# Optimization experiments

Hardware: AMD Instinct MI355X
Metric: run time of the kernel (lower is better)

## Reference

```python
import jax, jax.numpy as jnp
import numpy as np

N, G, F, K, E = 8192, 128, 128, 4, 1


def setup_inputs() -> dict:
    key = jax.random.key(0)
    k1, k2, k3, k4 = jax.random.split(key, 4)
    x = jax.random.normal(k1, (N, G), dtype=jnp.float32)
    # Scale GSO so repeated powers S^k stay numerically tame (spectral norm ~2).
    S = jax.random.normal(k2, (E, N, N), dtype=jnp.float32) / jnp.sqrt(jnp.float32(N))
    weight = jax.random.normal(k3, (F, E, K, G), dtype=jnp.float32)
    bias = jax.random.normal(k4, (F, 1), dtype=jnp.float32)
    return {"x": x, "S": S, "weight": weight, "bias": bias, "ind": 0}


def reference(x, S, weight, bias, ind):
    # x: [N, G] -> torch forward reshapes to [B=1, G, N]
    del ind  # GSO selector; the dense GSO S is passed in directly
    K_taps = weight.shape[2]
    Ef = S.shape[0]
    xk = jnp.broadcast_to(x.T[None, None], (1, Ef, x.shape[1], x.shape[0]))  # [B,E,G,N]
    zs = [xk]
    for _ in range(1, K_taps):  # fixed small K-hop power iteration
        xk = jnp.matmul(xk, S[None])  # [B,E,G,N] @ [1,E,N,N] -> [B,E,G,N]
        zs.append(xk)
    z = jnp.stack(zs, axis=2)  # [B,E,K,G,N]
    # y_f = sum_{e,k,g} h[f,e,k,g] * (S^k x)_g  + b_f
    y = jnp.einsum('bekgn,fekg->bfn', z, weight) + bias  # [B,F,N]
    return y
```

## Files before the change

### kernel.cpp

```cpp
#include <hip/hip_runtime.h>

typedef _Float16 f16;
typedef _Float16 f16x8 __attribute__((ext_vector_type(8)));
typedef float f32x4 __attribute__((ext_vector_type(4)));
typedef unsigned int u32;

#define NN 8192
#define GG 128
#define NSPLIT 16

typedef __attribute__((address_space(3))) unsigned as3u;
typedef const __attribute__((address_space(1))) unsigned as1u;

__device__ __forceinline__ void gload16(const f16* g, f16* l) {
  __builtin_amdgcn_global_load_lds((as1u*)g, (as3u*)l, 16, 0, 0);
}

#define SBAR() asm volatile("s_barrier" ::: "memory")
#define WAITV(N) asm volatile("s_waitcnt vmcnt(" #N ")" ::: "memory")
#define WAITL0() asm volatile("s_waitcnt lgkmcnt(0)" ::: "memory")

__device__ __forceinline__ f16x8 ldcvt8(const float* p) {
  f32x4 a = *(const f32x4*)p;
  f32x4 b = *(const f32x4*)(p + 4);
  f16x8 r;
  r[0] = (f16)a[0]; r[1] = (f16)a[1]; r[2] = (f16)a[2]; r[3] = (f16)a[3];
  r[4] = (f16)b[0]; r[5] = (f16)b[1]; r[6] = (f16)b[2]; r[7] = (f16)b[3];
  return r;
}

__global__ __launch_bounds__(512, 4) void k_cvtT(const float* __restrict__ S,
                                                 f16* __restrict__ Sbt) {
  const int tid = (int)threadIdx.x;
  const int w = tid >> 6, l = tid & 63;
  const int wid = (int)blockIdx.x * 8 + w;
  const int t = wid & 15;
  const int pair = (wid >> 4) & 31;
  const int split = wid >> 9;
  const int n0 = pair * 256;
  const int k0 = split * 512 + t * 32;

  const float* src = S + (size_t)k0 * NN + n0 + 4 * l;
  f16* chunk0 = Sbt + (((size_t)split * 64 + pair * 2) * 16 + t) * 4096;
  f16* chunkB = (l < 32) ? chunk0 : (chunk0 + 16 * 4096);
  const int c0 = (4 * l) & 127;

#pragma unroll
  for (int hi = 0; hi < 4; ++hi) {
    f32x4 v[8];
#pragma unroll
    for (int j = 0; j < 8; ++j)
      v[j] = __builtin_nontemporal_load((const f32x4*)(src + (size_t)(8 * hi + j) * NN));
#pragma unroll
    for (int i = 0; i < 4; ++i) {
      f16x8 h;
#pragma unroll
      for (int j = 0; j < 8; ++j) h[j] = (f16)v[j][i];
      const int c = c0 + i;
      const int unit = ((c >> 4) << 6) + (hi << 4) + (c & 15);
      *(f16x8*)(chunkB + (size_t)unit * 8) = h;
    }
  }
}

__global__ __launch_bounds__(512, 2) void k_wz(const float* __restrict__ wt,
                                               const float* __restrict__ x,
                                               f16* __restrict__ wz) {
  const int tid = (int)threadIdx.x;
  const int w = tid >> 6, l = tid & 63, lo = l & 15, hi = l >> 4;
  const int rg = w >> 1, cg = w & 1;
  const int ktap = (int)blockIdx.y;
  const int n0 = (int)blockIdx.x * 32;
  const int rowA = rg * 32;
  const float* wA0 = wt + (size_t)(rowA + lo) * 512 + (size_t)ktap * 128 + 8 * hi;
  const float* wA1 = wA0 + (size_t)16 * 512;
  const float* xB = x + (size_t)(n0 + 16 * cg + lo) * GG + 8 * hi;
  f32x4 acc[2] = {};
#pragma unroll
  for (int s = 0; s < 4; ++s) {
    f16x8 a0 = ldcvt8(wA0 + s * 32);
    f16x8 a1 = ldcvt8(wA1 + s * 32);
    f16x8 b = ldcvt8(xB + s * 32);
    acc[0] = __builtin_amdgcn_mfma_f32_16x16x32_f16(a0, b, acc[0], 0, 0, 0);
    acc[1] = __builtin_amdgcn_mfma_f32_16x16x32_f16(a1, b, acc[1], 0, 0, 0);
  }
  f16* out = wz + (size_t)ktap * (GG * NN);
#pragma unroll
  for (int fm = 0; fm < 2; ++fm)
#pragma unroll
    for (int rr = 0; rr < 4; ++rr) {
      int row = rowA + 16 * fm + 4 * hi + rr;
      out[(size_t)row * NN + n0 + 16 * cg + lo] = (f16)acc[fm][rr];
    }
}

__global__ __launch_bounds__(256, 3) void k_tapF(const f16* __restrict__ A,
                                                 const f16* __restrict__ Bt,
                                                 f16* __restrict__ Part) {
  __shared__ __align__(16) f16 sm[3 * 8192];

  const int tid = (int)threadIdx.x;
  const int w = tid >> 6, l = tid & 63, lo = l & 15, hi = l >> 4;
  const int wm = w >> 1, wn = w & 1;
  const int n0 = (int)blockIdx.x * 128;
  const int k0 = (int)blockIdx.y * 512;

  const int r1 = tid >> 2, r2 = 64 + (tid >> 2), q = tid & 3;
  const f16* aS1 = A + (size_t)r1 * NN + k0 + 8 * (q ^ (r1 & 3));
  const f16* aS2 = A + (size_t)r2 * NN + k0 + 8 * (q ^ (r2 & 3));
  const f16* bBlk = Bt + ((size_t)blockIdx.y * 64 + blockIdx.x) * (16 * 4096);

#pragma unroll
  for (int p = 0; p < 2; ++p) {
    f16* buf = sm + p * 8192;
    gload16(aS1 + p * 32, buf + tid * 8);
    gload16(aS2 + p * 32, buf + 2048 + tid * 8);
    gload16(bBlk + p * 4096 + tid * 8, buf + 4096 + tid * 8);
    gload16(bBlk + p * 4096 + 2048 + tid * 8, buf + 6144 + tid * 8);
  }

  f32x4 acc[4][4] = {};

  auto compute = [&](int cur) {
    const f16* Ab = sm + cur * 8192;
    const f16* Bb = Ab + 4096;
    f16x8 af[4], bf[4];
#pragma unroll
    for (int fm = 0; fm < 4; ++fm) {
      const int row = 64 * wm + 16 * fm + lo;
      af[fm] = *(const f16x8*)(Ab + row * 32 + 8 * (hi ^ (row & 3)));
    }
#pragma unroll
    for (int fn = 0; fn < 4; ++fn)
      bf[fn] = *(const f16x8*)(Bb + (wn * 4 + fn) * 512 + hi * 128 + lo * 8);
    WAITL0();
    __builtin_amdgcn_sched_barrier(0);
    __builtin_amdgcn_s_setprio(1);
#pragma unroll
    for (int fm = 0; fm < 4; ++fm)
#pragma unroll
      for (int fn = 0; fn < 4; ++fn)
        acc[fm][fn] = __builtin_amdgcn_mfma_f32_16x16x32_f16(af[fm], bf[fn], acc[fm][fn], 0, 0, 0);
    __builtin_amdgcn_s_setprio(0);
  };

  int cur = 0, nb = 2;
  for (int t = 0; t < 14; ++t) {
    f16* buf = sm + nb * 8192;
    const int ko = (t + 2) * 32;
    gload16(aS1 + ko, buf + tid * 8);
    gload16(aS2 + ko, buf + 2048 + tid * 8);
    gload16(bBlk + (size_t)(t + 2) * 4096 + tid * 8, buf + 4096 + tid * 8);
    gload16(bBlk + (size_t)(t + 2) * 4096 + 2048 + tid * 8, buf + 6144 + tid * 8);
    __builtin_amdgcn_sched_barrier(0);
    WAITV(8);
    SBAR();
    compute(cur);
    SBAR();
    cur = (cur == 2) ? 0 : cur + 1;
    nb = (nb == 2) ? 0 : nb + 1;
  }
  WAITV(4);
  SBAR();
  compute(cur);
  SBAR();
  cur = (cur == 2) ? 0 : cur + 1;
  WAITV(0);
  SBAR();
  compute(cur);

  f16* P = Part + (size_t)blockIdx.y * (GG * NN);
#pragma unroll
  for (int fm = 0; fm < 4; ++fm)
#pragma unroll
    for (int fn = 0; fn < 4; ++fn) {
      const int n = n0 + 64 * wn + 16 * fn + lo;
#pragma unroll
      for (int rr = 0; rr < 4; ++rr) {
        const int g = 64 * wm + 16 * fm + 4 * hi + rr;
        P[(size_t)g * NN + n] = (f16)acc[fm][fn][rr];
      }
    }
}

template <int FINAL>
__global__ void k_combine(const f16* __restrict__ Part, const f16* __restrict__ wz,
                          const float* __restrict__ bias, f16* __restrict__ tn,
                          float* __restrict__ y) {
  const int idx = (int)blockIdx.x * 512 + (int)threadIdx.x;
  const size_t off = (size_t)idx * 8;
  f16x8 wv = *(const f16x8*)(wz + off);
  float s[8];
#pragma unroll
  for (int j = 0; j < 8; ++j) s[j] = (float)wv[j];
#pragma unroll
  for (int sp = 0; sp < NSPLIT; ++sp) {
    f16x8 p = __builtin_nontemporal_load((const f16x8*)(Part + (size_t)sp * (GG * NN) + off));
#pragma unroll
    for (int j = 0; j < 8; ++j) s[j] += (float)p[j];
  }
  if (FINAL) {
    const float b = bias[(int)(off >> 13)];
    f32x4 o0, o1;
#pragma unroll
    for (int j = 0; j < 4; ++j) { o0[j] = s[j] + b; o1[j] = s[4 + j] + b; }
    *(f32x4*)(y + off) = o0;
    *(f32x4*)(y + off + 4) = o1;
  } else {
    f16x8 o;
#pragma unroll
    for (int j = 0; j < 8; ++j) o[j] = (f16)s[j];
    *(f16x8*)(tn + off) = o;
  }
}

extern "C" void kernel_launch(void* const* d_in, const int* in_sizes, int n_in, void* d_out,
                              int out_size, void* d_ws, size_t ws_size, hipStream_t stream) {
  const float* x = (const float*)d_in[0];
  const float* S = (const float*)d_in[1];
  const float* wt = (const float*)d_in[2];
  const float* bs = (const float*)d_in[3];
  float* y = (float*)d_out;
  char* ws = (char*)d_ws;

  const size_t offSbt = 0;
  const size_t offWz = offSbt + (size_t)NN * NN * 2;
  const size_t offTa = offWz + (size_t)4 * GG * NN * 2;
  const size_t offTb = offTa + (size_t)GG * NN * 2;
  const size_t offP = offTb + (size_t)GG * NN * 2;
  const size_t need = offP + (size_t)NSPLIT * GG * NN * 2;
  if (ws_size < need) return;

  f16* Sbt = (f16*)(ws + offSbt);
  f16* wz = (f16*)(ws + offWz);
  f16* ta = (f16*)(ws + offTa);
  f16* tb = (f16*)(ws + offTb);
  f16* Part = (f16*)(ws + offP);

  k_cvtT<<<dim3(1024), 512, 0, stream>>>(S, Sbt);
  k_wz<<<dim3(256, 4), 512, 0, stream>>>(wt, x, wz);

  k_tapF<<<dim3(64, NSPLIT), 256, 0, stream>>>(wz + (size_t)3 * GG * NN, Sbt, Part);
  k_combine<0><<<dim3(256), 512, 0, stream>>>(Part, wz + (size_t)2 * GG * NN, nullptr, ta, nullptr);
  k_tapF<<<dim3(64, NSPLIT), 256, 0, stream>>>(ta, Sbt, Part);
  k_combine<0><<<dim3(256), 512, 0, stream>>>(Part, wz + (size_t)1 * GG * NN, nullptr, tb, nullptr);
  k_tapF<<<dim3(64, NSPLIT), 256, 0, stream>>>(tb, Sbt, Part);
  k_combine<1><<<dim3(256), 512, 0, stream>>>(Part, wz, bs, nullptr, y);
}
```

Before: 207.7 us.

## Fuse S fp32-to-fp16 transpose into first tap GEMM and halve split-K

The separate conversion kernel that turned S from fp32 into a blocked fp16 layout is removed. The first tap GEMM now reads fp32 S directly, converts it in registers, writes it into LDS for its own MFMA use, and also writes it back to global memory for the later taps. Split-K drops from 16 to 8, so each block covers 1024 of K, which halves the partial-sum traffic in the combine kernels. In exchange there are fewer blocks per launch (512), and the first GEMM now has a heavier, hand-scheduled pipeline.

Result: faster. 171.4 us (-17.5%).

```diff
diff --git a/kernel.cpp b/kernel.cpp
--- a/kernel.cpp
+++ b/kernel.cpp
@@ -3,11 +3,10 @@
 typedef _Float16 f16;
 typedef _Float16 f16x8 __attribute__((ext_vector_type(8)));
 typedef float f32x4 __attribute__((ext_vector_type(4)));
-typedef unsigned int u32;
 
 #define NN 8192
 #define GG 128
-#define NSPLIT 16
+#define NSPLIT 8
 
 typedef __attribute__((address_space(3))) unsigned as3u;
 typedef const __attribute__((address_space(1))) unsigned as1u;
@@ -27,40 +26,6 @@
   r[0] = (f16)a[0]; r[1] = (f16)a[1]; r[2] = (f16)a[2]; r[3] = (f16)a[3];
   r[4] = (f16)b[0]; r[5] = (f16)b[1]; r[6] = (f16)b[2]; r[7] = (f16)b[3];
   return r;
-}
-
-__global__ __launch_bounds__(512, 4) void k_cvtT(const float* __restrict__ S,
-                                                 f16* __restrict__ Sbt) {
-  const int tid = (int)threadIdx.x;
-  const int w = tid >> 6, l = tid & 63;
-  const int wid = (int)blockIdx.x * 8 + w;
-  const int t = wid & 15;
-  const int pair = (wid >> 4) & 31;
-  const int split = wid >> 9;
-  const int n0 = pair * 256;
-  const int k0 = split * 512 + t * 32;
-
-  const float* src = S + (size_t)k0 * NN + n0 + 4 * l;
-  f16* chunk0 = Sbt + (((size_t)split * 64 + pair * 2) * 16 + t) * 4096;
-  f16* chunkB = (l < 32) ? chunk0 : (chunk0 + 16 * 4096);
-  const int c0 = (4 * l) & 127;
-
-#pragma unroll
-  for (int hi = 0; hi < 4; ++hi) {
-    f32x4 v[8];
-#pragma unroll
-    for (int j = 0; j < 8; ++j)
-      v[j] = __builtin_nontemporal_load((const f32x4*)(src + (size_t)(8 * hi + j) * NN));
-#pragma unroll
-    for (int i = 0; i < 4; ++i) {
-      f16x8 h;
-#pragma unroll
-      for (int j = 0; j < 8; ++j) h[j] = (f16)v[j][i];
-      const int c = c0 + i;
-      const int unit = ((c >> 4) << 6) + (hi << 4) + (c & 15);
-      *(f16x8*)(chunkB + (size_t)unit * 8) = h;
-    }
-  }
 }
 
 __global__ __launch_bounds__(512, 2) void k_wz(const float* __restrict__ wt,
@@ -94,6 +59,158 @@
     }
 }
 
+__global__ __launch_bounds__(256, 2) void k_tap1F(const f16* __restrict__ A,
+                                                  const float* __restrict__ S,
+                                                  f16* __restrict__ Sbt,
+                                                  f16* __restrict__ Part) {
+  __shared__ __align__(16) f16 sm[2 * 16384];
+
+  const int tid = (int)threadIdx.x;
+  const int w = tid >> 6, l = tid & 63, lo = l & 15, hi = l >> 4;
+  const int wm = w >> 1, wn = w & 1;
+  const int kg = tid >> 5, cg = tid & 31, ch = kg >> 2, khi = kg & 3;
+  const int nb = (int)blockIdx.x, ks = (int)blockIdx.y;
+  const int n0 = nb * 128;
+  const int k0 = ks * 1024;
+
+  const int r1 = tid >> 2, q = tid & 3;
+  const f16* aS1 = A + (size_t)r1 * NN + k0 + 8 * (q ^ (r1 & 3));
+  const f16* aS2 = A + (size_t)(64 + r1) * NN + k0 + 8 * (q ^ (r1 & 3));
+  const float* Sb = S + (size_t)(k0 + 8 * kg) * NN + n0 + 4 * cg;
+  f16* panel = Sbt + (size_t)(ks * 64 + nb) * (32 * 4096);
+
+  f32x4 rgA[8], rgB[8];
+  f32x4 acc[4][4] = {};
+
+#define ISSUE_R(T, RG)                                                          \
+  do {                                                                          \
+    const float* s_ = Sb + (size_t)(64 * (T)) * NN;                             \
+    _Pragma("unroll") for (int j_ = 0; j_ < 8; ++j_)                            \
+        RG[j_] = __builtin_nontemporal_load((const f32x4*)(s_ + (size_t)j_ * NN)); \
+  } while (0)
+
+#define ISSUE_G(T)                                                              \
+  do {                                                                          \
+    f16* bA_ = sm + ((T)&1) * 16384;                                            \
+    gload16(aS1 + 64 * (T), bA_ + tid * 8);                                     \
+    gload16(aS2 + 64 * (T), bA_ + 2048 + tid * 8);                              \
+    gload16(aS1 + 64 * (T) + 32, bA_ + 4096 + tid * 8);                         \
+    gload16(aS2 + 64 * (T) + 32, bA_ + 4096 + 2048 + tid * 8);                  \
+  } while (0)
+
+#define CVT_W(T, RG)                                                            \
+  do {                                                                          \
+    f16* bB_ = sm + ((T)&1) * 16384 + 8192 + ch * 4096;                         \
+    f16* g_ = panel + (size_t)(2 * (T) + ch) * 4096;                            \
+    _Pragma("unroll") for (int i_ = 0; i_ < 4; ++i_) {                          \
+      f16x8 h_;                                                                 \
+      _Pragma("unroll") for (int j_ = 0; j_ < 8; ++j_) h_[j_] = (f16)RG[j_][i_]; \
+      const int c_ = 4 * cg + i_;                                               \
+      const int u_ = ((c_ >> 4) << 6) + (khi << 4) + (c_ & 15);                 \
+      *(f16x8*)(bB_ + (size_t)(u_ ^ (cg >> 2)) * 8) = h_;                       \
+      *(f16x8*)(g_ + (size_t)u_ * 8) = h_;                                      \
+    }                                                                           \
+  } while (0)
+
+  auto compute2 = [&](int par) {
+    const f16* base = sm + par * 16384;
+#pragma unroll
+    for (int cc = 0; cc < 2; ++cc) {
+      const f16* Ab = base + cc * 4096;
+      const f16* Bb = base + 8192 + cc * 4096;
+      f16x8 af[4], bf[4];
+#pragma unroll
+      for (int fm = 0; fm < 4; ++fm) {
+        const int row = 64 * wm + 16 * fm + lo;
+        af[fm] = *(const f16x8*)(Ab + row * 32 + 8 * (hi ^ (row & 3)));
+      }
+#pragma unroll
+      for (int fn = 0; fn < 4; ++fn) {
+        const int uu = ((wn * 4 + fn) << 6) + (hi << 4) + lo;
+        bf[fn] = *(const f16x8*)(Bb + (size_t)(uu ^ (wn * 4 + fn)) * 8);
+      }
+      WAITL0();
+      __builtin_amdgcn_sched_barrier(0);
+      __builtin_amdgcn_s_setprio(1);
+#pragma unroll
+      for (int fm = 0; fm < 4; ++fm)
+#pragma unroll
+        for (int fn = 0; fn < 4; ++fn)
+          acc[fm][fn] = __builtin_amdgcn_mfma_f32_16x16x32_f16(af[fm], bf[fn], acc[fm][fn], 0, 0, 0);
+      __builtin_amdgcn_s_setprio(0);
+    }
+  };
+
+  ISSUE_R(0, rgA);
+  ISSUE_R(1, rgB);
+  ISSUE_G(0);
+  __builtin_amdgcn_sched_barrier(0);
+  WAITV(12);
+  __builtin_amdgcn_sched_barrier(0);
+  CVT_W(0, rgA);
+  __builtin_amdgcn_sched_barrier(0);
+
+  for (int tt = 0; tt < 7; ++tt) {
+    const int t0 = 2 * tt;
+    ISSUE_R(t0 + 2, rgA);
+    ISSUE_G(t0 + 1);
+    __builtin_amdgcn_sched_barrier(0);
+    WAITV(20);
+    __builtin_amdgcn_sched_barrier(0);
+    CVT_W(t0 + 1, rgB);
+    __builtin_amdgcn_sched_barrier(0);
+    WAITV(20);
+    WAITL0();
+    SBAR();
+    compute2(0);
+    SBAR();
+    ISSUE_R(t0 + 3, rgB);
+    ISSUE_G(t0 + 2);
+    __builtin_amdgcn_sched_barrier(0);
+    WAITV(20);
+    __builtin_amdgcn_sched_barrier(0);
+    CVT_W(t0 + 2, rgA);
+    __builtin_amdgcn_sched_barrier(0);
+    WAITV(20);
+    WAITL0();
+    SBAR();
+    compute2(1);
+    SBAR();
+  }
+  ISSUE_G(15);
+  __builtin_amdgcn_sched_barrier(0);
+  WAITV(12);
+  __builtin_amdgcn_sched_barrier(0);
+  CVT_W(15, rgB);
+  __builtin_amdgcn_sched_barrier(0);
+  WAITV(12);
+  WAITL0();
+  SBAR();
+  compute2(0);
+  SBAR();
+  WAITV(4);
+  __builtin_amdgcn_sched_barrier(0);
+  SBAR();
+  compute2(1);
+
+#undef ISSUE_R
+#undef ISSUE_G
+#undef CVT_W
+
+  f16* P = Part + (size_t)blockIdx.y * (GG * NN);
+#pragma unroll
+  for (int fm = 0; fm < 4; ++fm)
+#pragma unroll
+    for (int fn = 0; fn < 4; ++fn) {
+      const int n = n0 + 64 * wn + 16 * fn + lo;
+#pragma unroll
+      for (int rr = 0; rr < 4; ++rr) {
+        const int g = 64 * wm + 16 * fm + 4 * hi + rr;
+        P[(size_t)g * NN + n] = (f16)acc[fm][fn][rr];
+      }
+    }
+}
+
 __global__ __launch_bounds__(256, 3) void k_tapF(const f16* __restrict__ A,
                                                  const f16* __restrict__ Bt,
                                                  f16* __restrict__ Part) {
@@ -103,12 +220,12 @@
   const int w = tid >> 6, l = tid & 63, lo = l & 15, hi = l >> 4;
   const int wm = w >> 1, wn = w & 1;
   const int n0 = (int)blockIdx.x * 128;
-  const int k0 = (int)blockIdx.y * 512;
+  const int k0 = (int)blockIdx.y * 1024;
 
   const int r1 = tid >> 2, r2 = 64 + (tid >> 2), q = tid & 3;
   const f16* aS1 = A + (size_t)r1 * NN + k0 + 8 * (q ^ (r1 & 3));
   const f16* aS2 = A + (size_t)r2 * NN + k0 + 8 * (q ^ (r2 & 3));
-  const f16* bBlk = Bt + ((size_t)blockIdx.y * 64 + blockIdx.x) * (16 * 4096);
+  const f16* bBlk = Bt + (size_t)((int)blockIdx.y * 64 + (int)blockIdx.x) * (32 * 4096);
 
 #pragma unroll
   for (int p = 0; p < 2; ++p) {
@@ -145,7 +262,7 @@
   };
 
   int cur = 0, nb = 2;
-  for (int t = 0; t < 14; ++t) {
+  for (int t = 0; t < 30; ++t) {
     f16* buf = sm + nb * 8192;
     const int ko = (t + 2) * 32;
     gload16(aS1 + ko, buf + tid * 8);
@@ -237,10 +354,8 @@
   f16* tb = (f16*)(ws + offTb);
   f16* Part = (f16*)(ws + offP);
 
-  k_cvtT<<<dim3(1024), 512, 0, stream>>>(S, Sbt);
   k_wz<<<dim3(256, 4), 512, 0, stream>>>(wt, x, wz);
-
-  k_tapF<<<dim3(64, NSPLIT), 256, 0, stream>>>(wz + (size_t)3 * GG * NN, Sbt, Part);
+  k_tap1F<<<dim3(64, NSPLIT), 256, 0, stream>>>(wz + (size_t)3 * GG * NN, S, Sbt, Part);
   k_combine<0><<<dim3(256), 512, 0, stream>>>(Part, wz + (size_t)2 * GG * NN, nullptr, ta, nullptr);
   k_tapF<<<dim3(64, NSPLIT), 256, 0, stream>>>(ta, Sbt, Part);
   k_combine<0><<<dim3(256), 512, 0, stream>>>(Part, wz + (size_t)1 * GG * NN, nullptr, tb, nullptr);
```
